# Kernel tuning notes

Measured on AMD Instinct MI355X. Metric: run time of the kernel, lower is better.

## Reference

```python
import jax, jax.numpy as jnp
import numpy as np

NUM_HEAD = 8
DIM_MODEL = 512
DIM_HEAD = DIM_MODEL // NUM_HEAD
LN_EPS = 1e-5


def setup_inputs() -> dict:
    key = jax.random.key(0)
    ks = jax.random.split(key, 12)
    B, L, D = 4, 2048, DIM_MODEL
    s = 0.02
    return {
        "x": jax.random.normal(ks[0], (B, L, D), dtype=jnp.float32),
        "Wq": jax.random.normal(ks[1], (D, D), dtype=jnp.float32) * s,
        "bq": jnp.zeros((D,), dtype=jnp.float32),
        "Wk": jax.random.normal(ks[2], (D, D), dtype=jnp.float32) * s,
        "bk": jnp.zeros((D,), dtype=jnp.float32),
        "Wv": jax.random.normal(ks[3], (D, D), dtype=jnp.float32) * s,
        "bv": jnp.zeros((D,), dtype=jnp.float32),
        "Wo": jax.random.normal(ks[4], (D, D), dtype=jnp.float32) * s,
        "bo": jnp.zeros((D,), dtype=jnp.float32),
        "gamma": jnp.ones((D,), dtype=jnp.float32),
        "beta": jnp.zeros((D,), dtype=jnp.float32),
    }


def reference(x, Wq, bq, Wk, bk, Wv, bv, Wo, bo, gamma, beta):
    B, L, D = x.shape
    H, dh = NUM_HEAD, D // NUM_HEAD
    # QKV projections (torch Linear: x @ W.T + b)
    Q = x @ Wq.T + bq
    K = x @ Wk.T + bk
    V = x @ Wv.T + bv
    # Faithful to the torch code: contiguous view(B*H, L, dh)
    Q = Q.reshape(B * H, L, dh)
    K = K.reshape(B * H, L, dh)
    V = V.reshape(B * H, L, dh)
    scale = dh ** (-0.5)
    # [B*H, L, L] scores, scaled, softmax over keys
    attn = jax.nn.softmax(jnp.einsum("bqd,bkd->bqk", Q, K) * scale, axis=-1)
    context = jnp.einsum("bqk,bkd->bqd", attn, V)  # [B*H, L, dh]
    context = context.reshape(B, L, D)
    out = context @ Wo.T + bo
    out = out + x  # residual (dropout p=0.0 -> identity)
    # LayerNorm over last dim
    mu = jnp.mean(out, axis=-1, keepdims=True)
    var = jnp.mean(jnp.square(out - mu), axis=-1, keepdims=True)
    out = (out - mu) / jnp.sqrt(var + LN_EPS) * gamma + beta
    return out
```

## Files before the change

### kernel.cpp

```cpp
#include <hip/hip_runtime.h>

typedef __bf16 bf16;
typedef __bf16 bf16x4 __attribute__((ext_vector_type(4)));
typedef __bf16 bf16x8 __attribute__((ext_vector_type(8)));
typedef float f32x4 __attribute__((ext_vector_type(4)));

#define MFMA16(A, B, C) __builtin_amdgcn_mfma_f32_16x16x32_bf16((A), (B), (C), 0, 0, 0)

constexpr int Dm   = 512;
constexpr int Lm   = 2048;
constexpr int DH   = 64;
constexpr int Mrows = 8192;
constexpr int NHEADS = 32;

__global__ __launch_bounds__(256)
void cvt_kernel(const float* __restrict__ x, const float* __restrict__ Wq,
                const float* __restrict__ Wk, const float* __restrict__ Wv,
                const float* __restrict__ Wo,
                bf16* __restrict__ xb, bf16* __restrict__ Wqb, bf16* __restrict__ Wkb,
                bf16* __restrict__ Wvb, bf16* __restrict__ Wob)
{
    size_t i = ((size_t)blockIdx.x * 256 + threadIdx.x) * 4;
    const float* src; bf16* dst; size_t off;
    if (i < (size_t)Mrows * Dm) {
        src = x; dst = xb; off = i;
    } else {
        size_t r = i - (size_t)Mrows * Dm;
        int w = (int)(r >> 18);
        off = r & 262143;
        src = (w == 0) ? Wq : (w == 1) ? Wk : (w == 2) ? Wv : Wo;
        dst = (w == 0) ? Wqb : (w == 1) ? Wkb : (w == 2) ? Wvb : Wob;
    }
    float4 v = *reinterpret_cast<const float4*>(src + off);
    bf16x4 o; o[0] = (bf16)v.x; o[1] = (bf16)v.y; o[2] = (bf16)v.z; o[3] = (bf16)v.w;
    *reinterpret_cast<bf16x4*>(dst + off) = o;
}

__global__ __launch_bounds__(256)
void qkv_gemm(const bf16* __restrict__ xb,
              const bf16* __restrict__ Wqb, const float* __restrict__ bq,
              const bf16* __restrict__ Wkb, const float* __restrict__ bk,
              const bf16* __restrict__ Wvb, const float* __restrict__ bv,
              bf16* __restrict__ Qo, bf16* __restrict__ Ko, bf16* __restrict__ Vo)
{
    __shared__ bf16 Asm[128 * 40];
    __shared__ bf16 Bsm[128 * 40];

    const int z = blockIdx.z;
    const bf16* W = (z == 0) ? Wqb : (z == 1) ? Wkb : Wvb;
    const float* bias = (z == 0) ? bq : (z == 1) ? bk : bv;
    bf16* out = (z == 0) ? Qo : (z == 1) ? Ko : Vo;

    const int tid = threadIdx.x;
    const int row0 = blockIdx.y * 128;
    const int col0 = blockIdx.x * 128;

    const int srow = tid >> 1;
    const int skc  = (tid & 1) * 16;

    const int wv = tid >> 6;
    const int ln = tid & 63;
    const int wr = wv >> 1, wc = wv & 1;
    const int lr = ln & 15;
    const int lg = ln >> 4;

    f32x4 acc[4][4] = {};

    for (int kt = 0; kt < Dm; kt += 32) {
        __syncthreads();
        {
            const bf16* src = xb + (size_t)(row0 + srow) * Dm + kt + skc;
            *reinterpret_cast<bf16x8*>(&Asm[srow * 40 + skc])     = reinterpret_cast<const bf16x8*>(src)[0];
            *reinterpret_cast<bf16x8*>(&Asm[srow * 40 + skc + 8]) = reinterpret_cast<const bf16x8*>(src)[1];
        }
        {
            const bf16* src = W + (size_t)(col0 + srow) * Dm + kt + skc;
            *reinterpret_cast<bf16x8*>(&Bsm[srow * 40 + skc])     = reinterpret_cast<const bf16x8*>(src)[0];
            *reinterpret_cast<bf16x8*>(&Bsm[srow * 40 + skc + 8]) = reinterpret_cast<const bf16x8*>(src)[1];
        }
        __syncthreads();

        bf16x8 af[4], bfv[4];
        #pragma unroll
        for (int m = 0; m < 4; ++m)
            af[m] = *reinterpret_cast<const bf16x8*>(&Asm[(wr * 64 + m * 16 + lr) * 40 + lg * 8]);
        #pragma unroll
        for (int n = 0; n < 4; ++n)
            bfv[n] = *reinterpret_cast<const bf16x8*>(&Bsm[(wc * 64 + n * 16 + lr) * 40 + lg * 8]);
        #pragma unroll
        for (int m = 0; m < 4; ++m)
            #pragma unroll
            for (int n = 0; n < 4; ++n)
                acc[m][n] = MFMA16(af[m], bfv[n], acc[m][n]);
    }

    #pragma unroll
    for (int m = 0; m < 4; ++m)
        #pragma unroll
        for (int n = 0; n < 4; ++n)
            #pragma unroll
            for (int i = 0; i < 4; ++i) {
                int r = row0 + wr * 64 + m * 16 + lg * 4 + i;
                int c = col0 + wc * 64 + n * 16 + lr;
                out[(size_t)r * Dm + c] = (bf16)(acc[m][n][i] + bias[c]);
            }
}

__global__ __launch_bounds__(256)
void oproj_gemm(const bf16* __restrict__ ctx, const bf16* __restrict__ Wob,
                const float* __restrict__ bo, const float* __restrict__ x,
                float* __restrict__ tmp)
{
    __shared__ bf16 Asm[128 * 40];
    __shared__ bf16 Bsm[128 * 40];

    const int tid = threadIdx.x;
    const int row0 = blockIdx.y * 128;
    const int col0 = blockIdx.x * 128;

    const int srow = tid >> 1;
    const int skc  = (tid & 1) * 16;

    const int wv = tid >> 6;
    const int ln = tid & 63;
    const int wr = wv >> 1, wc = wv & 1;
    const int lr = ln & 15;
    const int lg = ln >> 4;

    f32x4 acc[4][4] = {};

    for (int kt = 0; kt < Dm; kt += 32) {
        __syncthreads();
        {
            const bf16* src = ctx + (size_t)(row0 + srow) * Dm + kt + skc;
            *reinterpret_cast<bf16x8*>(&Asm[srow * 40 + skc])     = reinterpret_cast<const bf16x8*>(src)[0];
            *reinterpret_cast<bf16x8*>(&Asm[srow * 40 + skc + 8]) = reinterpret_cast<const bf16x8*>(src)[1];
        }
        {
            const bf16* src = Wob + (size_t)(col0 + srow) * Dm + kt + skc;
            *reinterpret_cast<bf16x8*>(&Bsm[srow * 40 + skc])     = reinterpret_cast<const bf16x8*>(src)[0];
            *reinterpret_cast<bf16x8*>(&Bsm[srow * 40 + skc + 8]) = reinterpret_cast<const bf16x8*>(src)[1];
        }
        __syncthreads();

        bf16x8 af[4], bfv[4];
        #pragma unroll
        for (int m = 0; m < 4; ++m)
            af[m] = *reinterpret_cast<const bf16x8*>(&Asm[(wr * 64 + m * 16 + lr) * 40 + lg * 8]);
        #pragma unroll
        for (int n = 0; n < 4; ++n)
            bfv[n] = *reinterpret_cast<const bf16x8*>(&Bsm[(wc * 64 + n * 16 + lr) * 40 + lg * 8]);
        #pragma unroll
        for (int m = 0; m < 4; ++m)
            #pragma unroll
            for (int n = 0; n < 4; ++n)
                acc[m][n] = MFMA16(af[m], bfv[n], acc[m][n]);
    }

    #pragma unroll
    for (int m = 0; m < 4; ++m)
        #pragma unroll
        for (int n = 0; n < 4; ++n)
            #pragma unroll
            for (int i = 0; i < 4; ++i) {
                int r = row0 + wr * 64 + m * 16 + lg * 4 + i;
                int c = col0 + wc * 64 + n * 16 + lr;
                tmp[(size_t)r * Dm + c] = acc[m][n][i] + bo[c] + x[(size_t)r * Dm + c];
            }
}

__global__ __launch_bounds__(256)
void vt_kernel(const bf16* __restrict__ V, bf16* __restrict__ Vt)
{
    __shared__ bf16 T[64 * 72];
    const int head = blockIdx.y;
    const int k0 = blockIdx.x * 64;
    const size_t hb = (size_t)head * (Lm * DH);
    const int tid = threadIdx.x;
    const int r = tid >> 2;
    const int seg = (tid & 3) * 16;

    {
        const bf16* src = &V[hb + (size_t)(k0 + r) * DH + seg];
        *reinterpret_cast<bf16x8*>(&T[r * 72 + seg])     = reinterpret_cast<const bf16x8*>(src)[0];
        *reinterpret_cast<bf16x8*>(&T[r * 72 + seg + 8]) = reinterpret_cast<const bf16x8*>(src)[1];
    }
    __syncthreads();
    bf16 o[16];
    #pragma unroll
    for (int j = 0; j < 16; ++j) o[j] = T[(seg + j) * 72 + r];
    *reinterpret_cast<bf16x8*>(&Vt[hb + (size_t)r * Lm + k0 + seg])     = *reinterpret_cast<bf16x8*>(&o[0]);
    *reinterpret_cast<bf16x8*>(&Vt[hb + (size_t)r * Lm + k0 + seg + 8]) = *reinterpret_cast<bf16x8*>(&o[8]);
}

__global__ __launch_bounds__(256)
void flash_attn(const bf16* __restrict__ Q, const bf16* __restrict__ K,
                const bf16* __restrict__ Vt, bf16* __restrict__ ctx)
{
    __shared__ bf16 Ksm[64 * 72];
    __shared__ bf16 Vsm[64 * 72];
    __shared__ bf16 Psm[128 * 72];

    const int head = blockIdx.y;
    const int q0 = blockIdx.x * 128;
    const size_t hb = (size_t)head * (Lm * DH);

    const int tid = threadIdx.x;
    const int wv = tid >> 6;
    const int ln = tid & 63;
    const int lr = ln & 15;
    const int lg = ln >> 4;
    const int srow = tid >> 2;
    const int sseg = (tid & 3) * 16;

    const float qscale = 0.125f * 1.44269504088896340736f;
    bf16x8 qf[2][2];
    #pragma unroll
    for (int st = 0; st < 2; ++st) {
        const int qrow = q0 + wv * 32 + st * 16 + lr;
        #pragma unroll
        for (int s = 0; s < 2; ++s) {
            bf16x8 t = *reinterpret_cast<const bf16x8*>(&Q[hb + (size_t)qrow * DH + s * 32 + lg * 8]);
            #pragma unroll
            for (int j = 0; j < 8; ++j) qf[st][s][j] = (bf16)((float)t[j] * qscale);
        }
    }

    f32x4 cfr[2][4] = {};
    float lrow[2][4] = {};

    for (int k0 = 0; k0 < Lm; k0 += 64) {
        __syncthreads();
        {
            const bf16* src = &K[hb + (size_t)(k0 + srow) * DH + sseg];
            *reinterpret_cast<bf16x8*>(&Ksm[srow * 72 + sseg])     = reinterpret_cast<const bf16x8*>(src)[0];
            *reinterpret_cast<bf16x8*>(&Ksm[srow * 72 + sseg + 8]) = reinterpret_cast<const bf16x8*>(src)[1];
        }
        {
            const bf16* src = &Vt[hb + (size_t)srow * Lm + k0 + sseg];
            *reinterpret_cast<bf16x8*>(&Vsm[srow * 72 + sseg])     = reinterpret_cast<const bf16x8*>(src)[0];
            *reinterpret_cast<bf16x8*>(&Vsm[srow * 72 + sseg + 8]) = reinterpret_cast<const bf16x8*>(src)[1];
        }
        __syncthreads();

        #pragma unroll
        for (int st = 0; st < 2; ++st) {
            f32x4 sfr[4] = {};
            #pragma unroll
            for (int s = 0; s < 2; ++s)
                #pragma unroll
                for (int g = 0; g < 4; ++g) {
                    bf16x8 kf = *reinterpret_cast<const bf16x8*>(&Ksm[(g * 16 + lr) * 72 + s * 32 + lg * 8]);
                    sfr[g] = MFMA16(qf[st][s], kf, sfr[g]);
                }

            float rsum[4] = {0.f, 0.f, 0.f, 0.f};
            #pragma unroll
            for (int g = 0; g < 4; ++g)
                #pragma unroll
                for (int i = 0; i < 4; ++i) {
                    float p = exp2f(sfr[g][i]);
                    rsum[i] += p;
                    Psm[(wv * 32 + st * 16 + lg * 4 + i) * 72 + g * 16 + lr] = (bf16)p;
                }
            #pragma unroll
            for (int off = 1; off < 16; off <<= 1)
                #pragma unroll
                for (int i = 0; i < 4; ++i) rsum[i] += __shfl_xor(rsum[i], off);
            #pragma unroll
            for (int i = 0; i < 4; ++i) lrow[st][i] += rsum[i];
        }

        #pragma unroll
        for (int st = 0; st < 2; ++st)
            #pragma unroll
            for (int s = 0; s < 2; ++s) {
                bf16x8 pa = *reinterpret_cast<const bf16x8*>(&Psm[(wv * 32 + st * 16 + lr) * 72 + s * 32 + lg * 8]);
                #pragma unroll
                for (int n = 0; n < 4; ++n) {
                    bf16x8 vb = *reinterpret_cast<const bf16x8*>(&Vsm[(n * 16 + lr) * 72 + s * 32 + lg * 8]);
                    cfr[st][n] = MFMA16(pa, vb, cfr[st][n]);
                }
            }
    }

    #pragma unroll
    for (int st = 0; st < 2; ++st) {
        float inv[4];
        #pragma unroll
        for (int i = 0; i < 4; ++i) inv[i] = 1.f / lrow[st][i];
        #pragma unroll
        for (int n = 0; n < 4; ++n)
            #pragma unroll
            for (int i = 0; i < 4; ++i) {
                int q = q0 + wv * 32 + st * 16 + lg * 4 + i;
                int d = n * 16 + lr;
                ctx[hb + (size_t)q * DH + d] = (bf16)(cfr[st][n][i] * inv[i]);
            }
    }
}

__global__ __launch_bounds__(128)
void ln_kernel(const float* __restrict__ tmp, const float* __restrict__ gamma,
               const float* __restrict__ beta, float* __restrict__ out)
{
    const int row = blockIdx.x;
    const int tid = threadIdx.x;
    const int wv = tid >> 6;
    const int ln = tid & 63;

    float4 v = reinterpret_cast<const float4*>(tmp + (size_t)row * Dm)[tid];
    float s = v.x + v.y + v.z + v.w;
    float sq = v.x * v.x + v.y * v.y + v.z * v.z + v.w * v.w;

    #pragma unroll
    for (int off = 32; off > 0; off >>= 1) {
        s += __shfl_down(s, off);
        sq += __shfl_down(sq, off);
    }
    __shared__ float red[4];
    if (ln == 0) { red[wv * 2] = s; red[wv * 2 + 1] = sq; }
    __syncthreads();
    s = red[0] + red[2];
    sq = red[1] + red[3];

    const float mu = s * (1.f / Dm);
    const float var = sq * (1.f / Dm) - mu * mu;
    const float rstd = rsqrtf(var + 1e-5f);

    float4 g = reinterpret_cast<const float4*>(gamma)[tid];
    float4 b = reinterpret_cast<const float4*>(beta)[tid];
    float4 o;
    o.x = (v.x - mu) * rstd * g.x + b.x;
    o.y = (v.y - mu) * rstd * g.y + b.y;
    o.z = (v.z - mu) * rstd * g.z + b.z;
    o.w = (v.w - mu) * rstd * g.w + b.w;
    reinterpret_cast<float4*>(out + (size_t)row * Dm)[tid] = o;
}

extern "C" void kernel_launch(void* const* d_in, const int* in_sizes, int n_in,
                              void* d_out, int out_size, void* d_ws, size_t ws_size,
                              hipStream_t stream)
{
    const float* x  = (const float*)d_in[0];
    const float* Wq = (const float*)d_in[1];
    const float* bq = (const float*)d_in[2];
    const float* Wk = (const float*)d_in[3];
    const float* bk = (const float*)d_in[4];
    const float* Wv = (const float*)d_in[5];
    const float* bv = (const float*)d_in[6];
    const float* Wo = (const float*)d_in[7];
    const float* bo = (const float*)d_in[8];
    const float* gamma = (const float*)d_in[9];
    const float* beta  = (const float*)d_in[10];
    float* out = (float*)d_out;

    const size_t MD = (size_t)Mrows * Dm;
    const size_t WD = (size_t)Dm * Dm;
    char* p = (char*)d_ws;
    bf16* xb  = (bf16*)p;                 p += MD * 2;
    bf16* Qw  = (bf16*)p;                 p += MD * 2;
    bf16* Kw  = (bf16*)p;                 p += MD * 2;
    bf16* Vw  = (bf16*)p;                 p += MD * 2;
    bf16* Vtw = (bf16*)p;                 p += MD * 2;
    bf16* Wqb = (bf16*)p;                 p += WD * 2;
    bf16* Wkb = (bf16*)p;                 p += WD * 2;
    bf16* Wvb = (bf16*)p;                 p += WD * 2;
    bf16* Wob = (bf16*)p;                 p += WD * 2;
    float* Tw = (float*)d_ws;
    bf16* Cw = Vw;

    {
        const size_t total = MD + 4 * WD;
        cvt_kernel<<<dim3((unsigned)(total / (256 * 4))), 256, 0, stream>>>(
            x, Wq, Wk, Wv, Wo, xb, Wqb, Wkb, Wvb, Wob);
    }

    qkv_gemm<<<dim3(Dm / 128, Mrows / 128, 3), 256, 0, stream>>>(
        xb, Wqb, bq, Wkb, bk, Wvb, bv, Qw, Kw, Vw);

    vt_kernel<<<dim3(Lm / 64, NHEADS), 256, 0, stream>>>(Vw, Vtw);

    flash_attn<<<dim3(Lm / 128, NHEADS), 256, 0, stream>>>(Qw, Kw, Vtw, Cw);

    oproj_gemm<<<dim3(Dm / 128, Mrows / 128), 256, 0, stream>>>(Cw, Wob, bo, x, Tw);

    ln_kernel<<<dim3(Mrows), 128, 0, stream>>>(Tw, gamma, beta, out);
}
```

Measured before the change: 240.4 us.

## Use direct global-to-LDS loads in GEMMs and stream K/V from global in attention

Both projection GEMMs now stage A/B tiles with global_load_lds (16-byte direct-to-LDS loads) into an unpadded 32-wide layout instead of register round-trips into a padded one. The attention kernel drops K/V shared-memory staging and block barriers, reads K and Vt fragments straight from global/L2, and doubles the block to 512 threads with one 16-row query slice per wave. This trades barrier and LDS traffic for more global/L2 reads per wave. The unpadded LDS layout may also cause bank conflicts on the fragment reads. Psm is still written and read back within each wave without a barrier, which is safe only because each wave touches its own rows.

```diff
diff --git a/kernel.cpp b/kernel.cpp
--- a/kernel.cpp
+++ b/kernel.cpp
@@ -12,6 +12,12 @@
 constexpr int DH   = 64;
 constexpr int Mrows = 8192;
 constexpr int NHEADS = 32;
+
+__device__ __forceinline__ void gload16(const void* g, void* l) {
+    __builtin_amdgcn_global_load_lds(
+        (const __attribute__((address_space(1))) void*)g,
+        (__attribute__((address_space(3))) void*)l, 16, 0, 0);
+}
 
 __global__ __launch_bounds__(256)
 void cvt_kernel(const float* __restrict__ x, const float* __restrict__ Wq,
@@ -43,8 +49,8 @@
               const bf16* __restrict__ Wvb, const float* __restrict__ bv,
               bf16* __restrict__ Qo, bf16* __restrict__ Ko, bf16* __restrict__ Vo)
 {
-    __shared__ bf16 Asm[128 * 40];
-    __shared__ bf16 Bsm[128 * 40];
+    __shared__ bf16 Asm[128 * 32];
+    __shared__ bf16 Bsm[128 * 32];
 
     const int z = blockIdx.z;
     const bf16* W = (z == 0) ? Wqb : (z == 1) ? Wkb : Wvb;
@@ -54,9 +60,6 @@
     const int tid = threadIdx.x;
     const int row0 = blockIdx.y * 128;
     const int col0 = blockIdx.x * 128;
-
-    const int srow = tid >> 1;
-    const int skc  = (tid & 1) * 16;
 
     const int wv = tid >> 6;
     const int ln = tid & 63;
@@ -64,29 +67,30 @@
     const int lr = ln & 15;
     const int lg = ln >> 4;
 
+    const int srow = ln >> 2;
+    const int scol = (ln & 3) * 8;
+
     f32x4 acc[4][4] = {};
 
     for (int kt = 0; kt < Dm; kt += 32) {
         __syncthreads();
-        {
-            const bf16* src = xb + (size_t)(row0 + srow) * Dm + kt + skc;
-            *reinterpret_cast<bf16x8*>(&Asm[srow * 40 + skc])     = reinterpret_cast<const bf16x8*>(src)[0];
-            *reinterpret_cast<bf16x8*>(&Asm[srow * 40 + skc + 8]) = reinterpret_cast<const bf16x8*>(src)[1];
-        }
-        {
-            const bf16* src = W + (size_t)(col0 + srow) * Dm + kt + skc;
-            *reinterpret_cast<bf16x8*>(&Bsm[srow * 40 + skc])     = reinterpret_cast<const bf16x8*>(src)[0];
-            *reinterpret_cast<bf16x8*>(&Bsm[srow * 40 + skc + 8]) = reinterpret_cast<const bf16x8*>(src)[1];
+        #pragma unroll
+        for (int j = 0; j < 2; ++j) {
+            const int chunk = wv * 2 + j;
+            gload16(xb + (size_t)(row0 + chunk * 16 + srow) * Dm + kt + scol,
+                    &Asm[chunk * 512]);
+            gload16(W + (size_t)(col0 + chunk * 16 + srow) * Dm + kt + scol,
+                    &Bsm[chunk * 512]);
         }
         __syncthreads();
 
         bf16x8 af[4], bfv[4];
         #pragma unroll
         for (int m = 0; m < 4; ++m)
-            af[m] = *reinterpret_cast<const bf16x8*>(&Asm[(wr * 64 + m * 16 + lr) * 40 + lg * 8]);
+            af[m] = *reinterpret_cast<const bf16x8*>(&Asm[(wr * 64 + m * 16 + lr) * 32 + lg * 8]);
         #pragma unroll
         for (int n = 0; n < 4; ++n)
-            bfv[n] = *reinterpret_cast<const bf16x8*>(&Bsm[(wc * 64 + n * 16 + lr) * 40 + lg * 8]);
+            bfv[n] = *reinterpret_cast<const bf16x8*>(&Bsm[(wc * 64 + n * 16 + lr) * 32 + lg * 8]);
         #pragma unroll
         for (int m = 0; m < 4; ++m)
             #pragma unroll
@@ -111,15 +115,12 @@
                 const float* __restrict__ bo, const float* __restrict__ x,
                 float* __restrict__ tmp)
 {
-    __shared__ bf16 Asm[128 * 40];
-    __shared__ bf16 Bsm[128 * 40];
+    __shared__ bf16 Asm[128 * 32];
+    __shared__ bf16 Bsm[128 * 32];
 
     const int tid = threadIdx.x;
     const int row0 = blockIdx.y * 128;
     const int col0 = blockIdx.x * 128;
-
-    const int srow = tid >> 1;
-    const int skc  = (tid & 1) * 16;
 
     const int wv = tid >> 6;
     const int ln = tid & 63;
@@ -127,29 +128,30 @@
     const int lr = ln & 15;
     const int lg = ln >> 4;
 
+    const int srow = ln >> 2;
+    const int scol = (ln & 3) * 8;
+
     f32x4 acc[4][4] = {};
 
     for (int kt = 0; kt < Dm; kt += 32) {
         __syncthreads();
-        {
-            const bf16* src = ctx + (size_t)(row0 + srow) * Dm + kt + skc;
-            *reinterpret_cast<bf16x8*>(&Asm[srow * 40 + skc])     = reinterpret_cast<const bf16x8*>(src)[0];
-            *reinterpret_cast<bf16x8*>(&Asm[srow * 40 + skc + 8]) = reinterpret_cast<const bf16x8*>(src)[1];
-        }
-        {
-            const bf16* src = Wob + (size_t)(col0 + srow) * Dm + kt + skc;
-            *reinterpret_cast<bf16x8*>(&Bsm[srow * 40 + skc])     = reinterpret_cast<const bf16x8*>(src)[0];
-            *reinterpret_cast<bf16x8*>(&Bsm[srow * 40 + skc + 8]) = reinterpret_cast<const bf16x8*>(src)[1];
+        #pragma unroll
+        for (int j = 0; j < 2; ++j) {
+            const int chunk = wv * 2 + j;
+            gload16(ctx + (size_t)(row0 + chunk * 16 + srow) * Dm + kt + scol,
+                    &Asm[chunk * 512]);
+            gload16(Wob + (size_t)(col0 + chunk * 16 + srow) * Dm + kt + scol,
+                    &Bsm[chunk * 512]);
         }
         __syncthreads();
 
         bf16x8 af[4], bfv[4];
         #pragma unroll
         for (int m = 0; m < 4; ++m)
-            af[m] = *reinterpret_cast<const bf16x8*>(&Asm[(wr * 64 + m * 16 + lr) * 40 + lg * 8]);
+            af[m] = *reinterpret_cast<const bf16x8*>(&Asm[(wr * 64 + m * 16 + lr) * 32 + lg * 8]);
         #pragma unroll
         for (int n = 0; n < 4; ++n)
-            bfv[n] = *reinterpret_cast<const bf16x8*>(&Bsm[(wc * 64 + n * 16 + lr) * 40 + lg * 8]);
+            bfv[n] = *reinterpret_cast<const bf16x8*>(&Bsm[(wc * 64 + n * 16 + lr) * 32 + lg * 8]);
         #pragma unroll
         for (int m = 0; m < 4; ++m)
             #pragma unroll
@@ -193,12 +195,10 @@
     *reinterpret_cast<bf16x8*>(&Vt[hb + (size_t)r * Lm + k0 + seg + 8]) = *reinterpret_cast<bf16x8*>(&o[8]);
 }
 
-__global__ __launch_bounds__(256)
+__global__ __launch_bounds__(512)
 void flash_attn(const bf16* __restrict__ Q, const bf16* __restrict__ K,
                 const bf16* __restrict__ Vt, bf16* __restrict__ ctx)
 {
-    __shared__ bf16 Ksm[64 * 72];
-    __shared__ bf16 Vsm[64 * 72];
     __shared__ bf16 Psm[128 * 72];
 
     const int head = blockIdx.y;
@@ -210,94 +210,72 @@
     const int ln = tid & 63;
     const int lr = ln & 15;
     const int lg = ln >> 4;
-    const int srow = tid >> 2;
-    const int sseg = (tid & 3) * 16;
 
     const float qscale = 0.125f * 1.44269504088896340736f;
-    bf16x8 qf[2][2];
-    #pragma unroll
-    for (int st = 0; st < 2; ++st) {
-        const int qrow = q0 + wv * 32 + st * 16 + lr;
+    bf16x8 qf[2];
+    {
+        const int qrow = q0 + wv * 16 + lr;
         #pragma unroll
         for (int s = 0; s < 2; ++s) {
             bf16x8 t = *reinterpret_cast<const bf16x8*>(&Q[hb + (size_t)qrow * DH + s * 32 + lg * 8]);
             #pragma unroll
-            for (int j = 0; j < 8; ++j) qf[st][s][j] = (bf16)((float)t[j] * qscale);
-        }
-    }
-
-    f32x4 cfr[2][4] = {};
-    float lrow[2][4] = {};
+            for (int j = 0; j < 8; ++j) qf[s][j] = (bf16)((float)t[j] * qscale);
+        }
+    }
+
+    f32x4 cfr[4] = {};
+    float lrow[4] = {};
 
     for (int k0 = 0; k0 < Lm; k0 += 64) {
-        __syncthreads();
-        {
-            const bf16* src = &K[hb + (size_t)(k0 + srow) * DH + sseg];
-            *reinterpret_cast<bf16x8*>(&Ksm[srow * 72 + sseg])     = reinterpret_cast<const bf16x8*>(src)[0];
-            *reinterpret_cast<bf16x8*>(&Ksm[srow * 72 + sseg + 8]) = reinterpret_cast<const bf16x8*>(src)[1];
-        }
-        {
-            const bf16* src = &Vt[hb + (size_t)srow * Lm + k0 + sseg];
-            *reinterpret_cast<bf16x8*>(&Vsm[srow * 72 + sseg])     = reinterpret_cast<const bf16x8*>(src)[0];
-            *reinterpret_cast<bf16x8*>(&Vsm[srow * 72 + sseg + 8]) = reinterpret_cast<const bf16x8*>(src)[1];
-        }
-        __syncthreads();
-
-        #pragma unroll
-        for (int st = 0; st < 2; ++st) {
-            f32x4 sfr[4] = {};
-            #pragma unroll
-            for (int s = 0; s < 2; ++s)
-                #pragma unroll
-                for (int g = 0; g < 4; ++g) {
-                    bf16x8 kf = *reinterpret_cast<const bf16x8*>(&Ksm[(g * 16 + lr) * 72 + s * 32 + lg * 8]);
-                    sfr[g] = MFMA16(qf[st][s], kf, sfr[g]);
-                }
-
-            float rsum[4] = {0.f, 0.f, 0.f, 0.f};
-            #pragma unroll
-            for (int g = 0; g < 4; ++g)
-                #pragma unroll
-                for (int i = 0; i < 4; ++i) {
-                    float p = exp2f(sfr[g][i]);
-                    rsum[i] += p;
-                    Psm[(wv * 32 + st * 16 + lg * 4 + i) * 72 + g * 16 + lr] = (bf16)p;
-                }
-            #pragma unroll
-            for (int off = 1; off < 16; off <<= 1)
-                #pragma unroll
-                for (int i = 0; i < 4; ++i) rsum[i] += __shfl_xor(rsum[i], off);
-            #pragma unroll
-            for (int i = 0; i < 4; ++i) lrow[st][i] += rsum[i];
-        }
-
-        #pragma unroll
-        for (int st = 0; st < 2; ++st)
-            #pragma unroll
-            for (int s = 0; s < 2; ++s) {
-                bf16x8 pa = *reinterpret_cast<const bf16x8*>(&Psm[(wv * 32 + st * 16 + lr) * 72 + s * 32 + lg * 8]);
-                #pragma unroll
-                for (int n = 0; n < 4; ++n) {
-                    bf16x8 vb = *reinterpret_cast<const bf16x8*>(&Vsm[(n * 16 + lr) * 72 + s * 32 + lg * 8]);
-                    cfr[st][n] = MFMA16(pa, vb, cfr[st][n]);
-                }
-            }
-    }
-
-    #pragma unroll
-    for (int st = 0; st < 2; ++st) {
-        float inv[4];
-        #pragma unroll
-        for (int i = 0; i < 4; ++i) inv[i] = 1.f / lrow[st][i];
-        #pragma unroll
-        for (int n = 0; n < 4; ++n)
+        f32x4 sfr[4] = {};
+        #pragma unroll
+        for (int s = 0; s < 2; ++s)
+            #pragma unroll
+            for (int g = 0; g < 4; ++g) {
+                bf16x8 kf = *reinterpret_cast<const bf16x8*>(
+                    &K[hb + (size_t)(k0 + g * 16 + lr) * DH + s * 32 + lg * 8]);
+                sfr[g] = MFMA16(qf[s], kf, sfr[g]);
+            }
+
+        float rsum[4] = {0.f, 0.f, 0.f, 0.f};
+        #pragma unroll
+        for (int g = 0; g < 4; ++g)
             #pragma unroll
             for (int i = 0; i < 4; ++i) {
-                int q = q0 + wv * 32 + st * 16 + lg * 4 + i;
-                int d = n * 16 + lr;
-                ctx[hb + (size_t)q * DH + d] = (bf16)(cfr[st][n][i] * inv[i]);
-            }
-    }
+                float p = exp2f(sfr[g][i]);
+                rsum[i] += p;
+                Psm[(wv * 16 + lg * 4 + i) * 72 + g * 16 + lr] = (bf16)p;
+            }
+        #pragma unroll
+        for (int off = 1; off < 16; off <<= 1)
+            #pragma unroll
+            for (int i = 0; i < 4; ++i) rsum[i] += __shfl_xor(rsum[i], off);
+        #pragma unroll
+        for (int i = 0; i < 4; ++i) lrow[i] += rsum[i];
+
+        #pragma unroll
+        for (int s = 0; s < 2; ++s) {
+            bf16x8 pa = *reinterpret_cast<const bf16x8*>(&Psm[(wv * 16 + lr) * 72 + s * 32 + lg * 8]);
+            #pragma unroll
+            for (int n = 0; n < 4; ++n) {
+                bf16x8 vb = *reinterpret_cast<const bf16x8*>(
+                    &Vt[hb + (size_t)(n * 16 + lr) * Lm + k0 + s * 32 + lg * 8]);
+                cfr[n] = MFMA16(pa, vb, cfr[n]);
+            }
+        }
+    }
+
+    float inv[4];
+    #pragma unroll
+    for (int i = 0; i < 4; ++i) inv[i] = 1.f / lrow[i];
+    #pragma unroll
+    for (int n = 0; n < 4; ++n)
+        #pragma unroll
+        for (int i = 0; i < 4; ++i) {
+            int q = q0 + wv * 16 + lg * 4 + i;
+            int d = n * 16 + lr;
+            ctx[hb + (size_t)q * DH + d] = (bf16)(cfr[n][i] * inv[i]);
+        }
 }
 
 __global__ __launch_bounds__(128)
@@ -381,7 +359,7 @@
 
     vt_kernel<<<dim3(Lm / 64, NHEADS), 256, 0, stream>>>(Vw, Vtw);
 
-    flash_attn<<<dim3(Lm / 128, NHEADS), 256, 0, stream>>>(Qw, Kw, Vtw, Cw);
+    flash_attn<<<dim3(Lm / 128, NHEADS), 512, 0, stream>>>(Qw, Kw, Vtw, Cw);
 
     oproj_gemm<<<dim3(Dm / 128, Mrows / 128), 256, 0, stream>>>(Cw, Wob, bo, x, Tw);
 
```

After: 362.7 us. 1.51x slower.
